# Kernel optimization log

Hardware: AMD Instinct MI355X
Metric: run time of the kernel (lower is better)

## Reference

```python
import jax, jax.numpy as jnp
import numpy as np

# ---- static config (mirrors init_kwargs) ----
N_DIM = 3                      # manifold dimension n
D_COMP = 6                     # n(n+1)/2 metric components
M_PER = (12, 12, 12)           # HSGP basis functions per dim
M_STAR = 12 * 12 * 12          # 1728
T_STEPS = 50                   # time points in linspace(0,1,t)
C_SCALE = 1.5                  # HSGP domain scaling c
BATCH = 8192
ROWS = np.array([0, 1, 1, 2, 2, 2])   # lower-tri fill order of metric components
COLS = np.array([0, 0, 1, 0, 1, 2])


def _phi_dphi(x, L):
    """HSGP eigenfunctions and their spatial derivatives.
    x: [B, 3], L: [3] -> phi [B, M_STAR], dphi [B, M_STAR, 3]."""
    s, c = [], []
    for d in range(N_DIM):
        k = jnp.arange(1, M_PER[d] + 1, dtype=x.dtype)
        w = jnp.pi * k / (2.0 * L[d])                      # [m_d] frequencies
        arg = w[None, :] * (x[:, d:d + 1] + L[d])          # [B, m_d]
        scale = 1.0 / jnp.sqrt(L[d])
        s.append(scale * jnp.sin(arg))
        c.append(scale * jnp.cos(arg) * w[None, :])
    B = x.shape[0]
    phi = jnp.einsum('bi,bj,bk->bijk', s[0], s[1], s[2]).reshape(B, -1)
    d0 = jnp.einsum('bi,bj,bk->bijk', c[0], s[1], s[2]).reshape(B, -1)
    d1 = jnp.einsum('bi,bj,bk->bijk', s[0], c[1], s[2]).reshape(B, -1)
    d2 = jnp.einsum('bi,bj,bk->bijk', s[0], s[1], c[2]).reshape(B, -1)
    return phi, jnp.stack([d0, d1, d2], axis=-1)


def _omega(L):
    """[M_STAR, 3] angular frequencies of the tensor-product basis."""
    ks = [jnp.arange(1, m + 1, dtype=L.dtype) for m in M_PER]
    kg = jnp.stack(jnp.meshgrid(*ks, indexing='ij'), axis=-1).reshape(-1, N_DIM)
    return jnp.pi * kg / (2.0 * L[None, :])


def _metric_and_grad(x, W, L):
    """Metric g [B,3,3] and its spatial derivative dg [B,3,3,3] (last axis = d/dx_r)."""
    phi, dphi = _phi_dphi(x, L)
    gf = phi @ W.T                                   # [B, 6]
    dgf = jnp.einsum('bmr,dm->bdr', dphi, W)         # [B, 6, 3]
    B = x.shape[0]
    eye = jnp.eye(N_DIM, dtype=x.dtype)
    gl = jnp.zeros((B, N_DIM, N_DIM), x.dtype).at[:, ROWS, COLS].set(gf)
    g = gl + jnp.swapaxes(gl, 1, 2) - gl * eye + eye   # symmetrize + identity offset
    dgl = jnp.zeros((B, N_DIM, N_DIM, N_DIM), x.dtype).at[:, ROWS, COLS, :].set(dgf)
    dg = dgl + jnp.swapaxes(dgl, 1, 2) - dgl * eye[None, :, :, None]
    return g, dg


def _acceleration(pos, vel, W, L):
    """Geodesic equation: a^k = -Gamma^k_{ij} v^i v^j."""
    g, dg = _metric_and_grad(pos, W, L)
    ginv = jnp.linalg.inv(g)
    t1 = jnp.swapaxes(dg, 2, 3)            # [b,l,i,j] = d_i g_{lj}
    t3 = jnp.transpose(dg, (0, 3, 1, 2))   # [b,l,i,j] = d_l g_{ij}
    gamma = 0.5 * jnp.einsum('bkl,blij->bkij', ginv, t1 + dg - t3)
    return -jnp.einsum('bkij,bi,bj->bk', gamma, vel, vel)


def _integrate(pos0, vel0, W, L):
    dt = 1.0 / (T_STEPS - 1)

    def f(p, v):
        return v, _acceleration(p, v, W, L)

    def step(carry, _):
        p, v = carry
        dp1, dv1 = f(p, v)
        dp2, dv2 = f(p + 0.5 * dt * dp1, v + 0.5 * dt * dv1)
        dp3, dv3 = f(p + 0.5 * dt * dp2, v + 0.5 * dt * dv2)
        dp4, dv4 = f(p + dt * dp3, v + dt * dv3)
        pn = p + (dt / 6.0) * (dp1 + 2 * dp2 + 2 * dp3 + dp4)
        vn = v + (dt / 6.0) * (dv1 + 2 * dv2 + 2 * dv3 + dv4)
        return (pn, vn), (pn, vn)

    _, (ps, vs) = jax.lax.scan(step, (pos0, vel0), None, length=T_STEPS - 1)
    pos_traj = jnp.concatenate([pos0[None], ps], axis=0)   # [T, B, 3]
    vel_traj = jnp.concatenate([vel0[None], vs], axis=0)
    return jnp.stack([pos_traj, vel_traj], axis=1)          # [T, 2, B, 3]


def setup_inputs() -> dict:
    key = jax.random.key(0)
    k1, k2, k3, k4, k5 = jax.random.split(key, 5)
    return {
        'pos0': jax.random.normal(k1, (BATCH, N_DIM), jnp.float32),
        'vel0': jax.random.normal(k2, (BATCH, N_DIM), jnp.float32),
        'beta': 0.02 * jax.random.normal(k3, (D_COMP, M_STAR), jnp.float32),
        'ls': 0.5 + jax.random.uniform(k4, (D_COMP, N_DIM), jnp.float32),
        'basis': jax.random.normal(k5, (256, N_DIM), jnp.float32),
    }


def reference(pos0, vel0, beta, ls, basis):
    # HSGP domain half-widths from the linearization anchor points
    L = C_SCALE * jnp.max(jnp.abs(basis), axis=0)           # [3]
    om2 = _omega(L) ** 2                                     # [M_STAR, 3]
    # ExpQuad sqrt spectral density per GP component
    sqrt_psd = ((2.0 * jnp.pi) ** (N_DIM / 4.0)) \
        * jnp.sqrt(jnp.prod(ls, axis=1, keepdims=True)) \
        * jnp.exp(-0.25 * jnp.einsum('mi,di->dm', om2, ls ** 2))  # [6, M_STAR]
    W = beta * sqrt_psd                                      # [6, M_STAR]
    return _integrate(pos0, vel0, W, L)
```

## Files before the change

kernel.cpp:

```cpp
#include <hip/hip_runtime.h>
#include <hip/hip_bf16.h>
#include <math.h>

#define BATCH  8192
#define TSTEPS 50
#define PTS    32
#define LPP    24
#define NTHR   768
#define KDIM   144
#define KSTR   168
#define GKSTR  160
#define TSTR   100
#define NROW   96
#define PI_F   3.14159265358979323846f

typedef __bf16 bf16x8 __attribute__((ext_vector_type(8)));
typedef float  f32x4  __attribute__((ext_vector_type(4)));

__device__ __forceinline__ unsigned pack2bf(float a, float b) {
    unsigned short ua = __builtin_bit_cast(unsigned short, (__bf16)a);
    unsigned short ub = __builtin_bit_cast(unsigned short, (__bf16)b);
    return (unsigned)ua | ((unsigned)ub << 16);
}

__global__ void precompute_kernel(const float* __restrict__ beta,
                                  const float* __restrict__ ls,
                                  const float* __restrict__ basis,
                                  unsigned short* __restrict__ Wb,
                                  float* __restrict__ auxg)
{
    __shared__ float red[256];
    __shared__ float Ls[3], W1s[3];
    int t = threadIdx.x;

    for (int d = 0; d < 3; ++d) {
        red[t] = fabsf(basis[t*3 + d]);
        __syncthreads();
        for (int s = 128; s > 0; s >>= 1) {
            if (t < s) red[t] = fmaxf(red[t], red[t+s]);
            __syncthreads();
        }
        if (t == 0) {
            float L = 1.5f * red[0];
            Ls[d]  = L;
            W1s[d] = PI_F / (2.0f * L);
        }
        __syncthreads();
    }

    float pref[6], l20[6], l21[6], l22[6];
    #pragma unroll
    for (int dd = 0; dd < 6; ++dd) {
        float a = ls[dd*3+0], b = ls[dd*3+1], c = ls[dd*3+2];
        pref[dd] = 3.9685803f * sqrtf(a*b*c);
        l20[dd] = a*a; l21[dd] = b*b; l22[dd] = c*c;
    }

    for (int idx = t; idx < NROW*GKSTR; idx += 256) {
        int n = idx / GKSTR, k = idx - n*GKSTR;
        int d = n >> 4, i = n & 15;
        float v = 0.0f;
        if (i < 12 && k < KDIM) {
            int j = k / 12, kk = k - (k/12)*12;
            float o0 = W1s[0]*(float)(i+1);
            float o1 = W1s[1]*(float)(j+1);
            float o2 = W1s[2]*(float)(kk+1);
            float e = expf(-0.25f*(o0*o0*l20[d] + o1*o1*l21[d] + o2*o2*l22[d]));
            v = beta[d*1728 + i*144 + k] * pref[d] * e;
        }
        Wb[idx] = __builtin_bit_cast(unsigned short, (__bf16)v);
    }

    if (t < 3) {
        auxg[t]     = Ls[t];
        auxg[3 + t] = W1s[t];
        auxg[6 + t] = 1.0f / sqrtf(Ls[t]);
    }
}

__device__ __forceinline__ void eval_accel(
    float qx, float qy, float qz, float ux, float uy, float uz,
    const bf16x8* __restrict__ bfrag,
    __bf16* __restrict__ A, float* __restrict__ T,
    float (* __restrict__ tabs)[100], float (* __restrict__ scr)[28],
    const float* __restrict__ auxs,
    int tid, int pt, int role, int nt, int mb, int lrow, int lkg,
    float& ax, float& ay, float& az)
{
    {
        int first = (role < 12);
        int d  = first ? 0 : 1;
        int kk = first ? role : role - 12;
        float q = first ? qx : qy;
        float wk = auxs[3+d] * (float)(kk+1);
        float isq = auxs[6+d];
        float s, c;
        sincosf(wk*(q + auxs[d]), &s, &c);
        tabs[pt][d*24 + kk]      = isq*s;
        tabs[pt][d*24 + 12 + kk] = isq*c*wk;
        if (first) {
            float wk2 = auxs[5] * (float)(role+1);
            sincosf(wk2*(qz + auxs[2]), &s, &c);
            tabs[pt][48 + role] = auxs[8]*s;
            tabs[pt][60 + role] = auxs[8]*c*wk2;
        }
    }
    __syncthreads();

    {
        int j = role >> 1, kb = (role & 1)*6;
        float s1 = tabs[pt][24 + j], c1 = tabs[pt][36 + j];
        float s2v[6], c2v[6];
        #pragma unroll
        for (int u = 0; u < 6; ++u) {
            s2v[u] = tabs[pt][48 + kb + u];
            c2v[u] = tabs[pt][60 + kb + u];
        }
        unsigned* pss = (unsigned*)&A[(pt*3 + 0)*KSTR + role*6];
        unsigned* pcs = (unsigned*)&A[(pt*3 + 1)*KSTR + role*6];
        unsigned* psc = (unsigned*)&A[(pt*3 + 2)*KSTR + role*6];
        #pragma unroll
        for (int u = 0; u < 3; ++u) {
            pss[u] = pack2bf(s1*s2v[2*u], s1*s2v[2*u+1]);
            pcs[u] = pack2bf(c1*s2v[2*u], c1*s2v[2*u+1]);
            psc[u] = pack2bf(s1*c2v[2*u], s1*c2v[2*u+1]);
        }
        int zr = tid >> 3;
        *(unsigned*)&A[zr*KSTR + KDIM + ((tid & 7) << 1)] = 0u;
    }
    __syncthreads();

    f32x4 acc0 = {0.f,0.f,0.f,0.f}, acc1 = {0.f,0.f,0.f,0.f}, acc2 = {0.f,0.f,0.f,0.f};
    {
        #pragma unroll
        for (int ks = 0; ks < 5; ++ks) {
            int ko = ks*32 + lkg*8;
            bf16x8 a0 = *(const bf16x8*)&A[((mb+0)*16 + lrow)*KSTR + ko];
            bf16x8 a1 = *(const bf16x8*)&A[((mb+1)*16 + lrow)*KSTR + ko];
            bf16x8 a2 = *(const bf16x8*)&A[((mb+2)*16 + lrow)*KSTR + ko];
            acc0 = __builtin_amdgcn_mfma_f32_16x16x32_bf16(a0, bfrag[ks], acc0, 0, 0, 0);
            acc1 = __builtin_amdgcn_mfma_f32_16x16x32_bf16(a1, bfrag[ks], acc1, 0, 0, 0);
            acc2 = __builtin_amdgcn_mfma_f32_16x16x32_bf16(a2, bfrag[ks], acc2, 0, 0, 0);
        }
    }
    __syncthreads();
    {
        #pragma unroll
        for (int r = 0; r < 4; ++r) {
            T[((mb+0)*16 + lkg*4 + r)*TSTR + nt*16 + lrow] = acc0[r];
            T[((mb+1)*16 + lkg*4 + r)*TSTR + nt*16 + lrow] = acc1[r];
            T[((mb+2)*16 + lkg*4 + r)*TSTR + nt*16 + lrow] = acc2[r];
        }
    }
    __syncthreads();

    {
        int oi = role / 6, d = role - oi*6;
        int path = (oi <= 1) ? 0 : (oi - 1);
        int woff = (oi == 1) ? 12 : 0;
        const float* tr = &T[(pt*3 + path)*TSTR + d*16];
        const float* wr = &tabs[pt][woff];
        float s = 0.f;
        #pragma unroll
        for (int i = 0; i < 12; ++i) s = fmaf(wr[i], tr[i], s);
        scr[pt][role] = s;
    }
    __syncthreads();

    {
        const float* sp = scr[pt];
        float gfv[6], d0a[6], d1a[6], d2a[6];
        #pragma unroll
        for (int d = 0; d < 6; ++d) {
            gfv[d] = sp[d]; d0a[d] = sp[6+d]; d1a[d] = sp[12+d]; d2a[d] = sp[18+d];
        }
        float g00 = gfv[0]+1.f, g10 = gfv[1], g11 = gfv[2]+1.f;
        float g20 = gfv[3], g21 = gfv[4], g22 = gfv[5]+1.f;
        float a00 = g11*g22 - g21*g21;
        float a01 = g20*g21 - g10*g22;
        float a02 = g10*g21 - g20*g11;
        float a11 = g00*g22 - g20*g20;
        float a12 = g10*g20 - g00*g21;
        float a22 = g00*g11 - g10*g10;
        float det = g00*a00 + g10*a01 + g20*a02;
        float inv = 1.0f / det;
        float h00=a00*inv, h01=a01*inv, h02=a02*inv;
        float h11=a11*inv, h12=a12*inv, h22=a22*inv;

        float t0 = ux*d0a[0] + uy*d1a[0] + uz*d2a[0];
        float t1 = ux*d0a[1] + uy*d1a[1] + uz*d2a[1];
        float t2 = ux*d0a[2] + uy*d1a[2] + uz*d2a[2];
        float t3 = ux*d0a[3] + uy*d1a[3] + uz*d2a[3];
        float t4 = ux*d0a[4] + uy*d1a[4] + uz*d2a[4];
        float t5 = ux*d0a[5] + uy*d1a[5] + uz*d2a[5];

        float hl0 = ux*t0 + uy*t1 + uz*t3;
        float hl1 = ux*t1 + uy*t2 + uz*t4;
        float hl2 = ux*t3 + uy*t4 + uz*t5;

        float xx = ux*ux, yy = uy*uy, zz = uz*uz;
        float xy2 = 2.f*ux*uy, xz2 = 2.f*ux*uz, yz2 = 2.f*uy*uz;
        float e0 = xx*d0a[0] + xy2*d0a[1] + yy*d0a[2] + xz2*d0a[3] + yz2*d0a[4] + zz*d0a[5];
        float e1 = xx*d1a[0] + xy2*d1a[1] + yy*d1a[2] + xz2*d1a[3] + yz2*d1a[4] + zz*d1a[5];
        float e2 = xx*d2a[0] + xy2*d2a[1] + yy*d2a[2] + xz2*d2a[3] + yz2*d2a[4] + zz*d2a[5];

        float C0 = hl0 - 0.5f*e0;
        float C1 = hl1 - 0.5f*e1;
        float C2 = hl2 - 0.5f*e2;
        ax = -(h00*C0 + h01*C1 + h02*C2);
        ay = -(h01*C0 + h11*C1 + h12*C2);
        az = -(h02*C0 + h12*C1 + h22*C2);
    }
}

__global__ void __launch_bounds__(NTHR, 3) geodesic_kernel(
    const float* __restrict__ pos0, const float* __restrict__ vel0,
    const unsigned short* __restrict__ Wbg, const float* __restrict__ auxg,
    float* __restrict__ out)
{
    __shared__ __align__(16) unsigned char uni[NROW*TSTR*4];
    __shared__ __align__(16) float tabs[PTS][100];
    __shared__ __align__(16) float scr[PTS][28];
    __shared__ float auxs[9];

    __bf16* A = (__bf16*)uni;
    float*  T = (float*)uni;

    const int tid = threadIdx.x;
    if (tid < 9) auxs[tid] = auxg[tid];

    const int w = tid >> 6, lane = tid & 63;
    const int nt = w >> 1, mb = (w & 1) * 3;
    const int lrow = lane & 15, lkg = lane >> 4;

    bf16x8 bfrag[5];
    {
        const __bf16* Wb = (const __bf16*)Wbg;
        int n = nt*16 + lrow;
        #pragma unroll
        for (int ks = 0; ks < 5; ++ks)
            bfrag[ks] = *(const bf16x8*)(Wb + n*GKSTR + ks*32 + lkg*8);
    }

    const int pt   = tid / LPP;
    const int role = tid - pt*LPP;
    const int ptg  = blockIdx.x * PTS + pt;

    float px = pos0[ptg*3+0], py = pos0[ptg*3+1], pz = pos0[ptg*3+2];
    float vx = vel0[ptg*3+0], vy = vel0[ptg*3+1], vz = vel0[ptg*3+2];

    if (role < 3)      out[(size_t)ptg*3 + role] = (role==0)?px:((role==1)?py:pz);
    else if (role < 6) out[(size_t)BATCH*3 + (size_t)ptg*3 + (role-3)] = (role==3)?vx:((role==4)?vy:vz);

    __syncthreads();

    const float dt  = 1.0f/49.0f;
    const float hdt = 0.5f/49.0f;
    const float sdt = dt/6.0f;

    #pragma unroll 1
    for (int step = 0; step < TSTEPS-1; ++step) {
        float a1x,a1y,a1z, a2x,a2y,a2z, a3x,a3y,a3z, a4x,a4y,a4z;

        eval_accel(px,py,pz, vx,vy,vz, bfrag, A, T, tabs, scr, auxs,
                   tid, pt, role, nt, mb, lrow, lkg, a1x,a1y,a1z);

        float p2x = fmaf(hdt,vx,px), p2y = fmaf(hdt,vy,py), p2z = fmaf(hdt,vz,pz);
        float v2x = fmaf(hdt,a1x,vx), v2y = fmaf(hdt,a1y,vy), v2z = fmaf(hdt,a1z,vz);
        eval_accel(p2x,p2y,p2z, v2x,v2y,v2z, bfrag, A, T, tabs, scr, auxs,
                   tid, pt, role, nt, mb, lrow, lkg, a2x,a2y,a2z);

        float p3x = fmaf(hdt,v2x,px), p3y = fmaf(hdt,v2y,py), p3z = fmaf(hdt,v2z,pz);
        float v3x = fmaf(hdt,a2x,vx), v3y = fmaf(hdt,a2y,vy), v3z = fmaf(hdt,a2z,vz);
        eval_accel(p3x,p3y,p3z, v3x,v3y,v3z, bfrag, A, T, tabs, scr, auxs,
                   tid, pt, role, nt, mb, lrow, lkg, a3x,a3y,a3z);

        float p4x = fmaf(dt,v3x,px), p4y = fmaf(dt,v3y,py), p4z = fmaf(dt,v3z,pz);
        float v4x = fmaf(dt,a3x,vx), v4y = fmaf(dt,a3y,vy), v4z = fmaf(dt,a3z,vz);
        eval_accel(p4x,p4y,p4z, v4x,v4y,v4z, bfrag, A, T, tabs, scr, auxs,
                   tid, pt, role, nt, mb, lrow, lkg, a4x,a4y,a4z);

        px = px + sdt*(vx + 2.f*v2x + 2.f*v3x + v4x);
        py = py + sdt*(vy + 2.f*v2y + 2.f*v3y + v4y);
        pz = pz + sdt*(vz + 2.f*v2z + 2.f*v3z + v4z);
        vx = vx + sdt*(a1x + 2.f*a2x + 2.f*a3x + a4x);
        vy = vy + sdt*(a1y + 2.f*a2y + 2.f*a3y + a4y);
        vz = vz + sdt*(a1z + 2.f*a2z + 2.f*a3z + a4z);

        size_t ob = (size_t)(step+1) * 2u * BATCH * 3u;
        if (role < 3)      out[ob + (size_t)ptg*3 + role] = (role==0)?px:((role==1)?py:pz);
        else if (role < 6) out[ob + (size_t)BATCH*3 + (size_t)ptg*3 + (role-3)] = (role==3)?vx:((role==4)?vy:vz);
    }
}

extern "C" void kernel_launch(void* const* d_in, const int* in_sizes, int n_in,
                              void* d_out, int out_size, void* d_ws, size_t ws_size,
                              hipStream_t stream) {
    (void)in_sizes; (void)n_in; (void)out_size; (void)ws_size;
    const float* pos0  = (const float*)d_in[0];
    const float* vel0  = (const float*)d_in[1];
    const float* beta  = (const float*)d_in[2];
    const float* ls    = (const float*)d_in[3];
    const float* basis = (const float*)d_in[4];
    float* outp = (float*)d_out;

    unsigned short* Wb = (unsigned short*)d_ws;
    float* auxg = (float*)((char*)d_ws + NROW*GKSTR*sizeof(unsigned short));

    precompute_kernel<<<1, 256, 0, stream>>>(beta, ls, basis, Wb, auxg);
    geodesic_kernel<<<256, NTHR, 0, stream>>>(pos0, vel0, Wb, auxg, outp);
}
```

Baseline: 514.6 us.

## Transpose MFMA roles and fuse basis contraction into register epilogue with shuffles

```diff
diff --git a/kernel.cpp b/kernel.cpp
--- a/kernel.cpp
+++ b/kernel.cpp
@@ -1,5 +1,4 @@
 #include <hip/hip_runtime.h>
-#include <hip/hip_bf16.h>
 #include <math.h>
 
 #define BATCH  8192
@@ -7,10 +6,9 @@
 #define PTS    32
 #define LPP    24
 #define NTHR   768
-#define KDIM   144
 #define KSTR   168
 #define GKSTR  160
-#define TSTR   100
+#define TABSTR 100
 #define NROW   96
 #define PI_F   3.14159265358979323846f
 
@@ -60,7 +58,7 @@
         int n = idx / GKSTR, k = idx - n*GKSTR;
         int d = n >> 4, i = n & 15;
         float v = 0.0f;
-        if (i < 12 && k < KDIM) {
+        if (i < 12 && k < 144) {
             int j = k / 12, kk = k - (k/12)*12;
             float o0 = W1s[0]*(float)(i+1);
             float o1 = W1s[1]*(float)(j+1);
@@ -80,102 +78,107 @@
 
 __device__ __forceinline__ void eval_accel(
     float qx, float qy, float qz, float ux, float uy, float uz,
-    const bf16x8* __restrict__ bfrag,
-    __bf16* __restrict__ A, float* __restrict__ T,
-    float (* __restrict__ tabs)[100], float (* __restrict__ scr)[28],
-    const float* __restrict__ auxs,
-    int tid, int pt, int role, int nt, int mb, int lrow, int lkg,
+    const bf16x8 (* __restrict__ wfrag)[5],
+    __bf16* __restrict__ P, float (* __restrict__ tabs)[TABSTR],
+    float (* __restrict__ scr)[28],
+    float L0, float L1, float L2, float w10, float w11, float w12,
+    float isq0, float isq1, float isq2,
+    int pt, int role, int mb, int lrow, int lkg, int nn, int ptn, int pn,
     float& ax, float& ay, float& az)
 {
-    {
-        int first = (role < 12);
-        int d  = first ? 0 : 1;
-        int kk = first ? role : role - 12;
-        float q = first ? qx : qy;
-        float wk = auxs[3+d] * (float)(kk+1);
-        float isq = auxs[6+d];
+    if (role < 12) {
         float s, c;
-        sincosf(wk*(q + auxs[d]), &s, &c);
-        tabs[pt][d*24 + kk]      = isq*s;
-        tabs[pt][d*24 + 12 + kk] = isq*c*wk;
-        if (first) {
-            float wk2 = auxs[5] * (float)(role+1);
-            sincosf(wk2*(qz + auxs[2]), &s, &c);
-            tabs[pt][48 + role] = auxs[8]*s;
-            tabs[pt][60 + role] = auxs[8]*c*wk2;
-        }
+        float wk = w10 * (float)(role+1);
+        __sincosf(wk*(qx + L0), &s, &c);
+        tabs[pt][role]      = isq0*s;
+        tabs[pt][16 + role] = isq0*c*wk;
+        float wk2 = w12 * (float)(role+1);
+        __sincosf(wk2*(qz + L2), &s, &c);
+        tabs[pt][56 + role] = isq2*s;
+        tabs[pt][68 + role] = isq2*c*wk2;
+    } else {
+        int kk = role - 12;
+        float s, c;
+        float wk = w11 * (float)(kk+1);
+        __sincosf(wk*(qy + L1), &s, &c);
+        tabs[pt][32 + kk] = isq1*s;
+        tabs[pt][44 + kk] = isq1*c*wk;
     }
     __syncthreads();
 
     {
         int j = role >> 1, kb = (role & 1)*6;
-        float s1 = tabs[pt][24 + j], c1 = tabs[pt][36 + j];
+        float s1 = tabs[pt][32 + j], c1 = tabs[pt][44 + j];
         float s2v[6], c2v[6];
         #pragma unroll
         for (int u = 0; u < 6; ++u) {
-            s2v[u] = tabs[pt][48 + kb + u];
-            c2v[u] = tabs[pt][60 + kb + u];
-        }
-        unsigned* pss = (unsigned*)&A[(pt*3 + 0)*KSTR + role*6];
-        unsigned* pcs = (unsigned*)&A[(pt*3 + 1)*KSTR + role*6];
-        unsigned* psc = (unsigned*)&A[(pt*3 + 2)*KSTR + role*6];
+            s2v[u] = tabs[pt][56 + kb + u];
+            c2v[u] = tabs[pt][68 + kb + u];
+        }
+        int colb = j*12 + kb;
+        unsigned* pss = (unsigned*)&P[(pt*3 + 0)*KSTR + colb];
+        unsigned* pcs = (unsigned*)&P[(pt*3 + 1)*KSTR + colb];
+        unsigned* psc = (unsigned*)&P[(pt*3 + 2)*KSTR + colb];
         #pragma unroll
         for (int u = 0; u < 3; ++u) {
             pss[u] = pack2bf(s1*s2v[2*u], s1*s2v[2*u+1]);
             pcs[u] = pack2bf(c1*s2v[2*u], c1*s2v[2*u+1]);
             psc[u] = pack2bf(s1*c2v[2*u], s1*c2v[2*u+1]);
         }
-        int zr = tid >> 3;
-        *(unsigned*)&A[zr*KSTR + KDIM + ((tid & 7) << 1)] = 0u;
     }
     __syncthreads();
 
     f32x4 acc0 = {0.f,0.f,0.f,0.f}, acc1 = {0.f,0.f,0.f,0.f}, acc2 = {0.f,0.f,0.f,0.f};
+    #pragma unroll
+    for (int ks = 0; ks < 5; ++ks) {
+        bf16x8 pf = *(const bf16x8*)&P[nn*KSTR + ks*32 + lkg*8];
+        acc0 = __builtin_amdgcn_mfma_f32_16x16x32_bf16(wfrag[0][ks], pf, acc0, 0, 0, 0);
+        acc1 = __builtin_amdgcn_mfma_f32_16x16x32_bf16(wfrag[1][ks], pf, acc1, 0, 0, 0);
+        acc2 = __builtin_amdgcn_mfma_f32_16x16x32_bf16(wfrag[2][ks], pf, acc2, 0, 0, 0);
+    }
+
     {
-        #pragma unroll
-        for (int ks = 0; ks < 5; ++ks) {
-            int ko = ks*32 + lkg*8;
-            bf16x8 a0 = *(const bf16x8*)&A[((mb+0)*16 + lrow)*KSTR + ko];
-            bf16x8 a1 = *(const bf16x8*)&A[((mb+1)*16 + lrow)*KSTR + ko];
-            bf16x8 a2 = *(const bf16x8*)&A[((mb+2)*16 + lrow)*KSTR + ko];
-            acc0 = __builtin_amdgcn_mfma_f32_16x16x32_bf16(a0, bfrag[ks], acc0, 0, 0, 0);
-            acc1 = __builtin_amdgcn_mfma_f32_16x16x32_bf16(a1, bfrag[ks], acc1, 0, 0, 0);
-            acc2 = __builtin_amdgcn_mfma_f32_16x16x32_bf16(a2, bfrag[ks], acc2, 0, 0, 0);
+        f32x4 s0v = *(const f32x4*)&tabs[ptn][lkg*4];
+        f32x4 c0v = *(const f32x4*)&tabs[ptn][16 + lkg*4];
+
+        float vs0 = acc0[0]*s0v[0] + acc0[1]*s0v[1] + acc0[2]*s0v[2] + acc0[3]*s0v[3];
+        float vs1 = acc1[0]*s0v[0] + acc1[1]*s0v[1] + acc1[2]*s0v[2] + acc1[3]*s0v[3];
+        float vs2 = acc2[0]*s0v[0] + acc2[1]*s0v[1] + acc2[2]*s0v[2] + acc2[3]*s0v[3];
+        float vc0 = acc0[0]*c0v[0] + acc0[1]*c0v[1] + acc0[2]*c0v[2] + acc0[3]*c0v[3];
+        float vc1 = acc1[0]*c0v[0] + acc1[1]*c0v[1] + acc1[2]*c0v[2] + acc1[3]*c0v[3];
+        float vc2 = acc2[0]*c0v[0] + acc2[1]*c0v[1] + acc2[2]*c0v[2] + acc2[3]*c0v[3];
+
+        vs0 += __shfl_xor(vs0, 16); vs0 += __shfl_xor(vs0, 32);
+        vs1 += __shfl_xor(vs1, 16); vs1 += __shfl_xor(vs1, 32);
+        vs2 += __shfl_xor(vs2, 16); vs2 += __shfl_xor(vs2, 32);
+        vc0 += __shfl_xor(vc0, 16); vc0 += __shfl_xor(vc0, 32);
+        vc1 += __shfl_xor(vc1, 16); vc1 += __shfl_xor(vc1, 32);
+        vc2 += __shfl_xor(vc2, 16); vc2 += __shfl_xor(vc2, 32);
+
+        if (lkg == 0) {
+            int off = (pn == 0) ? 0 : ((pn == 1) ? 12 : 18);
+            scr[ptn][off + mb + 0] = vs0;
+            scr[ptn][off + mb + 1] = vs1;
+            scr[ptn][off + mb + 2] = vs2;
+        }
+        if (lkg == 1 && pn == 0) {
+            scr[ptn][6 + mb + 0] = vc0;
+            scr[ptn][6 + mb + 1] = vc1;
+            scr[ptn][6 + mb + 2] = vc2;
         }
     }
     __syncthreads();
+
     {
-        #pragma unroll
-        for (int r = 0; r < 4; ++r) {
-            T[((mb+0)*16 + lkg*4 + r)*TSTR + nt*16 + lrow] = acc0[r];
-            T[((mb+1)*16 + lkg*4 + r)*TSTR + nt*16 + lrow] = acc1[r];
-            T[((mb+2)*16 + lkg*4 + r)*TSTR + nt*16 + lrow] = acc2[r];
-        }
-    }
-    __syncthreads();
-
-    {
-        int oi = role / 6, d = role - oi*6;
-        int path = (oi <= 1) ? 0 : (oi - 1);
-        int woff = (oi == 1) ? 12 : 0;
-        const float* tr = &T[(pt*3 + path)*TSTR + d*16];
-        const float* wr = &tabs[pt][woff];
-        float s = 0.f;
-        #pragma unroll
-        for (int i = 0; i < 12; ++i) s = fmaf(wr[i], tr[i], s);
-        scr[pt][role] = s;
-    }
-    __syncthreads();
-
-    {
-        const float* sp = scr[pt];
-        float gfv[6], d0a[6], d1a[6], d2a[6];
-        #pragma unroll
-        for (int d = 0; d < 6; ++d) {
-            gfv[d] = sp[d]; d0a[d] = sp[6+d]; d1a[d] = sp[12+d]; d2a[d] = sp[18+d];
-        }
-        float g00 = gfv[0]+1.f, g10 = gfv[1], g11 = gfv[2]+1.f;
-        float g20 = gfv[3], g21 = gfv[4], g22 = gfv[5]+1.f;
+        const f32x4* sp = (const f32x4*)&scr[pt][0];
+        f32x4 q0 = sp[0], q1 = sp[1], q2 = sp[2], q3 = sp[3], q4 = sp[4], q5 = sp[5];
+
+        float g00 = q0[0]+1.f, g10 = q0[1], g11 = q0[2]+1.f;
+        float g20 = q0[3], g21 = q1[0], g22 = q1[1]+1.f;
+        float d0a0=q1[2], d0a1=q1[3], d0a2=q2[0], d0a3=q2[1], d0a4=q2[2], d0a5=q2[3];
+        float d1a0=q3[0], d1a1=q3[1], d1a2=q3[2], d1a3=q3[3], d1a4=q4[0], d1a5=q4[1];
+        float d2a0=q4[2], d2a1=q4[3], d2a2=q5[0], d2a3=q5[1], d2a4=q5[2], d2a5=q5[3];
+
         float a00 = g11*g22 - g21*g21;
         float a01 = g20*g21 - g10*g22;
         float a02 = g10*g21 - g20*g11;
@@ -187,12 +190,12 @@
         float h00=a00*inv, h01=a01*inv, h02=a02*inv;
         float h11=a11*inv, h12=a12*inv, h22=a22*inv;
 
-        float t0 = ux*d0a[0] + uy*d1a[0] + uz*d2a[0];
-        float t1 = ux*d0a[1] + uy*d1a[1] + uz*d2a[1];
-        float t2 = ux*d0a[2] + uy*d1a[2] + uz*d2a[2];
-        float t3 = ux*d0a[3] + uy*d1a[3] + uz*d2a[3];
-        float t4 = ux*d0a[4] + uy*d1a[4] + uz*d2a[4];
-        float t5 = ux*d0a[5] + uy*d1a[5] + uz*d2a[5];
+        float t0 = ux*d0a0 + uy*d1a0 + uz*d2a0;
+        float t1 = ux*d0a1 + uy*d1a1 + uz*d2a1;
+        float t2 = ux*d0a2 + uy*d1a2 + uz*d2a2;
+        float t3 = ux*d0a3 + uy*d1a3 + uz*d2a3;
+        float t4 = ux*d0a4 + uy*d1a4 + uz*d2a4;
+        float t5 = ux*d0a5 + uy*d1a5 + uz*d2a5;
 
         float hl0 = ux*t0 + uy*t1 + uz*t3;
         float hl1 = ux*t1 + uy*t2 + uz*t4;
@@ -200,9 +203,9 @@
 
         float xx = ux*ux, yy = uy*uy, zz = uz*uz;
         float xy2 = 2.f*ux*uy, xz2 = 2.f*ux*uz, yz2 = 2.f*uy*uz;
-        float e0 = xx*d0a[0] + xy2*d0a[1] + yy*d0a[2] + xz2*d0a[3] + yz2*d0a[4] + zz*d0a[5];
-        float e1 = xx*d1a[0] + xy2*d1a[1] + yy*d1a[2] + xz2*d1a[3] + yz2*d1a[4] + zz*d1a[5];
-        float e2 = xx*d2a[0] + xy2*d2a[1] + yy*d2a[2] + xz2*d2a[3] + yz2*d2a[4] + zz*d2a[5];
+        float e0 = xx*d0a0 + xy2*d0a1 + yy*d0a2 + xz2*d0a3 + yz2*d0a4 + zz*d0a5;
+        float e1 = xx*d1a0 + xy2*d1a1 + yy*d1a2 + xz2*d1a3 + yz2*d1a4 + zz*d1a5;
+        float e2 = xx*d2a0 + xy2*d2a1 + yy*d2a2 + xz2*d2a3 + yz2*d2a4 + zz*d2a5;
 
         float C0 = hl0 - 0.5f*e0;
         float C1 = hl1 - 0.5f*e1;
@@ -218,28 +221,36 @@
     const unsigned short* __restrict__ Wbg, const float* __restrict__ auxg,
     float* __restrict__ out)
 {
-    __shared__ __align__(16) unsigned char uni[NROW*TSTR*4];
-    __shared__ __align__(16) float tabs[PTS][100];
+    __shared__ __align__(16) __bf16 P[NROW*KSTR];
+    __shared__ __align__(16) float tabs[PTS][TABSTR];
     __shared__ __align__(16) float scr[PTS][28];
-    __shared__ float auxs[9];
-
-    __bf16* A = (__bf16*)uni;
-    float*  T = (float*)uni;
 
     const int tid = threadIdx.x;
-    if (tid < 9) auxs[tid] = auxg[tid];
+
+    for (int idx = tid; idx < NROW*KSTR/2; idx += NTHR) ((unsigned*)P)[idx] = 0u;
+    if (tid < PTS*8) {
+        int zp = tid >> 3, s = tid & 7;
+        tabs[zp][(s < 4) ? (12 + s) : (24 + s)] = 0.f;
+    }
+
+    float L0 = auxg[0], L1 = auxg[1], L2 = auxg[2];
+    float w10 = auxg[3], w11 = auxg[4], w12 = auxg[5];
+    float isq0 = auxg[6], isq1 = auxg[7], isq2 = auxg[8];
 
     const int w = tid >> 6, lane = tid & 63;
     const int nt = w >> 1, mb = (w & 1) * 3;
     const int lrow = lane & 15, lkg = lane >> 4;
-
-    bf16x8 bfrag[5];
+    const int nn = nt*16 + lrow;
+    const int ptn = nn / 3, pn = nn - 3*ptn;
+
+    bf16x8 wfrag[3][5];
     {
         const __bf16* Wb = (const __bf16*)Wbg;
-        int n = nt*16 + lrow;
         #pragma unroll
-        for (int ks = 0; ks < 5; ++ks)
-            bfrag[ks] = *(const bf16x8*)(Wb + n*GKSTR + ks*32 + lkg*8);
+        for (int mt = 0; mt < 3; ++mt)
+            #pragma unroll
+            for (int ks = 0; ks < 5; ++ks)
+                wfrag[mt][ks] = *(const bf16x8*)(Wb + ((mb+mt)*16 + lrow)*GKSTR + ks*32 + lkg*8);
     }
 
     const int pt   = tid / LPP;
@@ -262,23 +273,27 @@
     for (int step = 0; step < TSTEPS-1; ++step) {
         float a1x,a1y,a1z, a2x,a2y,a2z, a3x,a3y,a3z, a4x,a4y,a4z;
 
-        eval_accel(px,py,pz, vx,vy,vz, bfrag, A, T, tabs, scr, auxs,
-                   tid, pt, role, nt, mb, lrow, lkg, a1x,a1y,a1z);
+        eval_accel(px,py,pz, vx,vy,vz, wfrag, P, tabs, scr,
+                   L0,L1,L2,w10,w11,w12,isq0,isq1,isq2,
+                   pt, role, mb, lrow, lkg, nn, ptn, pn, a1x,a1y,a1z);
 
         float p2x = fmaf(hdt,vx,px), p2y = fmaf(hdt,vy,py), p2z = fmaf(hdt,vz,pz);
         float v2x = fmaf(hdt,a1x,vx), v2y = fmaf(hdt,a1y,vy), v2z = fmaf(hdt,a1z,vz);
-        eval_accel(p2x,p2y,p2z, v2x,v2y,v2z, bfrag, A, T, tabs, scr, auxs,
-                   tid, pt, role, nt, mb, lrow, lkg, a2x,a2y,a2z);
+        eval_accel(p2x,p2y,p2z, v2x,v2y,v2z, wfrag, P, tabs, scr,
+                   L0,L1,L2,w10,w11,w12,isq0,isq1,isq2,
+                   pt, role, mb, lrow, lkg, nn, ptn, pn, a2x,a2y,a2z);
 
         float p3x = fmaf(hdt,v2x,px), p3y = fmaf(hdt,v2y,py), p3z = fmaf(hdt,v2z,pz);
         float v3x = fmaf(hdt,a2x,vx), v3y = fmaf(hdt,a2y,vy), v3z = fmaf(hdt,a2z,vz);
-        eval_accel(p3x,p3y,p3z, v3x,v3y,v3z, bfrag, A, T, tabs, scr, auxs,
-                   tid, pt, role, nt, mb, lrow, lkg, a3x,a3y,a3z);
+        eval_accel(p3x,p3y,p3z, v3x,v3y,v3z, wfrag, P, tabs, scr,
+                   L0,L1,L2,w10,w11,w12,isq0,isq1,isq2,
+                   pt, role, mb, lrow, lkg, nn, ptn, pn, a3x,a3y,a3z);
 
         float p4x = fmaf(dt,v3x,px), p4y = fmaf(dt,v3y,py), p4z = fmaf(dt,v3z,pz);
         float v4x = fmaf(dt,a3x,vx), v4y = fmaf(dt,a3y,vy), v4z = fmaf(dt,a3z,vz);
-        eval_accel(p4x,p4y,p4z, v4x,v4y,v4z, bfrag, A, T, tabs, scr, auxs,
-                   tid, pt, role, nt, mb, lrow, lkg, a4x,a4y,a4z);
+        eval_accel(p4x,p4y,p4z, v4x,v4y,v4z, wfrag, P, tabs, scr,
+                   L0,L1,L2,w10,w11,w12,isq0,isq1,isq2,
+                   pt, role, mb, lrow, lkg, nn, ptn, pn, a4x,a4y,a4z);
 
         px = px + sdt*(vx + 2.f*v2x + 2.f*v3x + v4x);
         py = py + sdt*(vy + 2.f*v2y + 2.f*v3y + v4y);
```

After: 428.0 us. 1.2x faster.
